# Kernel optimization log

Measured on AMD Instinct MI355X. Metric: run time of the kernel, lower is better.

## Reference

```python
import jax, jax.numpy as jnp
import numpy as np

N_WIRES = 16
VAR_DEPTH = 2
BATCH = 16


def _param_sizes():
    sizes = []
    n = N_WIRES
    lay = 0
    while n > 1:
        sizes.append(4 * int(np.ceil(N_WIRES / 2 ** lay)) * VAR_DEPTH)
        n = (n + 1) // 2
        lay += 1
    return sizes  # [128, 64, 32, 16]


def _apply_1q(psi, gate, w):
    # psi: (B, 2, ..., 2); gate: (2,2) complex; wire w lives on axis w+1
    psi = jnp.moveaxis(psi, w + 1, -1)
    psi = jnp.einsum('...j,ij->...i', psi, gate)
    return jnp.moveaxis(psi, -1, w + 1)


def _rx(psi, th, w):
    c = jnp.cos(th / 2).astype(jnp.complex64)
    s = jnp.sin(th / 2).astype(jnp.complex64)
    gate = jnp.stack([jnp.stack([c, -1j * s]), jnp.stack([-1j * s, c])])
    return _apply_1q(psi, gate, w)


def _rz(psi, th, w):
    ph = jnp.exp(0.5j * th * jnp.array([-1.0, 1.0], jnp.float32)).astype(jnp.complex64)
    shape = [1] * psi.ndim
    shape[w + 1] = 2
    return psi * ph.reshape(shape)


def _rzz(psi, th, wa, wb):
    # diag(e^{-i t/2}, e^{i t/2}, e^{i t/2}, e^{-i t/2}) -> sign = -1 if bits equal else +1
    sgn = jnp.array([[-1.0, 1.0], [1.0, -1.0]], jnp.float32)
    ph = jnp.exp(0.5j * th * sgn).astype(jnp.complex64)  # symmetric, transpose-safe
    a, b = min(wa, wb) + 1, max(wa, wb) + 1
    shape = [1] * psi.ndim
    shape[a] = 2
    shape[b] = 2
    return psi * ph.reshape(shape)


def _cnot(psi, c, t):
    p0 = jax.lax.slice_in_dim(psi, 0, 1, axis=c + 1)
    p1 = jax.lax.slice_in_dim(psi, 1, 2, axis=c + 1)
    return jnp.concatenate([p0, jnp.flip(p1, axis=t + 1)], axis=c + 1)


def _conv_layer(psi, params, active):
    n = len(active)
    for d in range(VAR_DEPTH):
        for j in range(n):
            base = 4 * j + d * 4 * n
            psi = _rx(psi, params[base + 0], active[j])
            psi = _rz(psi, params[base + 1], active[j])
            psi = _rx(psi, params[base + 2], active[j])
        for bg in (0, 1):
            for j in range(bg, n, 2):
                jn = (j + 1) % n  # ring coupling (wraps last->first)
                base = 4 * j + d * 4 * n
                psi = _rzz(psi, params[base + 3], active[j], active[jn])
    return psi


def _pool(psi, active):
    for j in range(0, len(active), 2):
        if j + 1 < len(active):
            psi = _cnot(psi, active[j], active[j + 1])
    return psi, active[::2]


def _forward(psi, params_list):
    active = list(range(N_WIRES))
    for p in params_list:
        psi = _conv_layer(psi, p, active)
        if len(active) > 1:
            psi, active = _pool(psi, active)
    w = active[0]  # measure Z on the surviving wire (wire 0)
    prob = psi.real ** 2 + psi.imag ** 2
    axes = tuple(a for a in range(1, psi.ndim) if a != w + 1)
    p2 = prob.sum(axis=axes)  # (B, 2)
    return p2[:, 0] - p2[:, 1]


def setup_inputs() -> dict:
    key = jax.random.key(0)
    ks = jax.random.split(key, 8)
    dim = 2 ** N_WIRES
    x_re = jax.random.normal(ks[0], (BATCH, dim), dtype=jnp.float32)
    x_im = jax.random.normal(ks[1], (BATCH, dim), dtype=jnp.float32)
    nrm = jnp.sqrt(jnp.sum(x_re ** 2 + x_im ** 2, axis=1, keepdims=True))
    x_re = x_re / nrm
    x_im = x_im / nrm
    sizes = _param_sizes()
    two_pi = 2.0 * np.pi
    params = [jax.random.uniform(ks[2 + i], (sizes[i],), dtype=jnp.float32) * two_pi
              for i in range(len(sizes))]
    return {"x_re": x_re, "x_im": x_im,
            "params0": params[0], "params1": params[1],
            "params2": params[2], "params3": params[3]}


def reference(x_re, x_im, params0, params1, params2, params3):
    psi = (x_re + 1j * x_im).astype(jnp.complex64)
    psi = psi.reshape((BATCH,) + (2,) * N_WIRES)
    return _forward(psi, [params0, params1, params2, params3])
```

## Files before the change

kernel.cpp:

```cpp
#include <hip/hip_runtime.h>


#define DEV __device__ __forceinline__

__device__ static const unsigned char G_CP[60] = {
  15,14,13,12,11,10,9,8,7,6,5,4,3,2,1,0,
  15,14,13,12,11,10,9,8,7,6,5,4,3,2,1,0,
  15,13,11,9,7,5,3,1,
  15,13,11,9,7,5,3,1,
  15,11,7,3,
  15,11,7,3,
  15,7,
  15,7
};
__device__ static const unsigned char G_CQ[60] = {
  14,13,12,11,10,9,8,7,6,5,4,3,2,1,0,15,
  14,13,12,11,10,9,8,7,6,5,4,3,2,1,0,15,
  13,11,9,7,5,3,1,15,
  13,11,9,7,5,3,1,15,
  11,7,3,15,
  11,7,3,15,
  7,15,
  7,15
};

DEV float2 F2(float x, float y){ float2 r; r.x = x; r.y = y; return r; }
DEV float2 cmulf(float2 a, float2 b){ return F2(a.x*b.x - a.y*b.y, a.x*b.y + a.y*b.x); }
DEV int swz(int j){ return j ^ ((j>>4)&15) ^ ((j>>8)&15); }

#if __has_builtin(__builtin_amdgcn_permlane32_swap)
#define HAVE_PLS 1
DEV void plswap01(float &x0, float &x1){
  auto r = __builtin_amdgcn_permlane32_swap(__float_as_uint(x0), __float_as_uint(x1), false, false);
  x0 = __uint_as_float((unsigned)r[0]);
  x1 = __uint_as_float((unsigned)r[1]);
}
#else
#define HAVE_PLS 0
#endif

template<int SB>
DEV void gate4(float2* a, const float* __restrict__ g){
  float u00r=g[0],u00i=g[1],u01r=g[2],u01i=g[3],u10r=g[4],u10i=g[5],u11r=g[6],u11i=g[7];
  #pragma unroll
  for (int m=0;m<2;m++){
    int i0 = (SB==0) ? (m<<1) : m;
    int i1 = i0 | (1<<SB);
    float2 x0=a[i0], x1=a[i1];
    a[i0] = F2(u00r*x0.x - u00i*x0.y + u01r*x1.x - u01i*x1.y,
               u00r*x0.y + u00i*x0.x + u01r*x1.y + u01i*x1.x);
    a[i1] = F2(u10r*x0.x - u10i*x0.y + u11r*x1.x - u11i*x1.y,
               u10r*x0.y + u10i*x0.x + u11r*x1.y + u11i*x1.x);
  }
}

DEV void lgate(float2* a, const float* __restrict__ g, int mask, int lane){
  bool h = (lane & mask) != 0;
  float Ar = h ? g[6] : g[0], Ai = h ? g[7] : g[1];
  float Br = h ? g[4] : g[2], Bi = h ? g[5] : g[3];
  #pragma unroll
  for (int s=0;s<4;s++){
    float px = __shfl_xor(a[s].x, mask);
    float py = __shfl_xor(a[s].y, mask);
    a[s] = F2(Ar*a[s].x - Ai*a[s].y + Br*px - Bi*py,
              Ar*a[s].y + Ai*a[s].x + Br*py + Bi*px);
  }
}

DEV void lgate32(float2* a, const float* __restrict__ g, int lane){
#if HAVE_PLS
  bool h = (lane & 32) != 0;
  float c0r = h ? g[4] : g[0], c0i = h ? g[5] : g[1];
  float c1r = h ? g[6] : g[2], c1i = h ? g[7] : g[3];
  #pragma unroll
  for (int s=0;s<4;s++){
    float x0x = a[s].x, x1x = a[s].x, x0y = a[s].y, x1y = a[s].y;
    plswap01(x0x, x1x); plswap01(x0y, x1y);
    a[s] = F2(c0r*x0x - c0i*x0y + c1r*x1x - c1i*x1y,
              c0r*x0y + c0i*x0x + c1r*x1y + c1i*x1x);
  }
#else
  lgate(a, g, 32, lane);
#endif
}

DEV void cswap(float2* a, int cmask, int tmask, int lane){
  bool c = (lane & cmask) != 0;
  #pragma unroll
  for (int s=0;s<4;s++){
    float px = __shfl_xor(a[s].x, tmask);
    float py = __shfl_xor(a[s].y, tmask);
    if (c){ a[s].x = px; a[s].y = py; }
  }
}

template<int C0,int N,unsigned M0,unsigned M1>
DEV void diag4(float2* a, const float* __restrict__ hh, unsigned Ib){
  const unsigned regmask = M0|M1;
  float base = 0.f;
  #pragma unroll
  for (int k=0;k<N;k++){
    const int p = G_CP[C0+k], q = G_CQ[C0+k];
    if ( !(((1u<<p)|(1u<<q)) & regmask) ){
      float h = hh[C0+k];
      unsigned x = ((Ib>>p) ^ (Ib>>q)) & 1u;
      base += x ? h : -h;
    }
  }
  #pragma unroll
  for (int r=0;r<4;r++){
    unsigned Ir = Ib ^ ((r&1)?M0:0u) ^ ((r&2)?M1:0u);
    float ph = base;
    #pragma unroll
    for (int k=0;k<N;k++){
      const int p = G_CP[C0+k], q = G_CQ[C0+k];
      if ( ((1u<<p)|(1u<<q)) & regmask ){
        float h = hh[C0+k];
        unsigned x = ((Ir>>p) ^ (Ir>>q)) & 1u;
        ph += x ? h : -h;
      }
    }
    float c, s;
    __sincosf(ph, &s, &c);
    a[r] = cmulf(a[r], F2(c, s));
  }
}

DEV void build_entry(float* sh, const float* __restrict__ p0, const float* __restrict__ p1,
                     const float* __restrict__ p2, const float* __restrict__ p3, int g){
  int d, j, n; const float* P;
  if (g < 32)      { n=16; d=(g>>4)&1; j=g&15; P=p0; }
  else if (g < 48) { n=8;  d=(g>>3)&1; j=g&7;  P=p1; }
  else if (g < 56) { n=4;  d=(g>>2)&1; j=g&3;  P=p2; }
  else             { n=2;  d=(g>>1)&1; j=g&1;  P=p3; }
  int base = 4*j + 4*n*d;
  float th0 = P[base+0], th1 = P[base+1], th2 = P[base+2], th3 = P[base+3];
  float c0,s0,ca,sa,c2,s2;
  sincosf(0.5f*th0, &s0, &c0);
  sincosf(0.5f*th1, &sa, &ca);
  sincosf(0.5f*th2, &s2, &c2);
  float B00r =  ca*c0, B00i = -sa*c0;
  float B01r = -sa*s0, B01i = -ca*s0;
  float B10r =  sa*s0, B10i = -ca*s0;
  float B11r =  ca*c0, B11i =  sa*c0;
  float* o8 = sh + g*8;
  o8[0]=c2*B00r + s2*B10i; o8[1]=c2*B00i - s2*B10r;
  o8[2]=c2*B01r + s2*B11i; o8[3]=c2*B01i - s2*B11r;
  o8[4]=s2*B00i + c2*B10r; o8[5]=-s2*B00r + c2*B10i;
  o8[6]=s2*B01i + c2*B11r; o8[7]=-s2*B01r + c2*B11i;
  sh[480 + g] = 0.5f*th3;
}

DEV unsigned Ib2(int j, int o){ return (unsigned)((j&63) | (o<<6) | ((j>>6)<<11)); }
DEV unsigned Ic(int j, int o){
  return (unsigned)( ((j&1)<<1) | (((j>>1)&1)<<3) | (((j>>2)&1)<<5)
       | (((j>>3)&63)<<6) | (((j>>9)&1)<<13) | (((j>>10)&1)<<15)
       | (o&1) | (((o>>1)&1)<<2) | (((o>>2)&1)<<4) | (((o>>3)&1)<<12) | (((o>>4)&1)<<14) );
}
DEV unsigned s1b(unsigned I){ return I ^ ((I & 0xA02Au) >> 1); }

__global__ __launch_bounds__(512, 4)
void k_p1(const float* __restrict__ xre, const float* __restrict__ xim,
          const float* __restrict__ pp0, const float* __restrict__ pp1,
          const float* __restrict__ pp2, const float* __restrict__ pp3,
          float* __restrict__ tbl, float2* __restrict__ st, float* __restrict__ out){
  const int t = threadIdx.x, lane = t & 63, wv = t >> 6;
  const int batch = blockIdx.x >> 5, o = blockIdx.x & 31;
  const unsigned hi = ((unsigned)batch<<16) | ((unsigned)o<<11);
  __shared__ float2 lds[2048];
  __shared__ float sh[544];
  float2 a[4];
  {
    unsigned base = hi | ((unsigned)t<<2);
    float4 re = *(const float4*)(xre + base);
    float4 im = *(const float4*)(xim + base);
    a[0]=F2(re.x,im.x); a[1]=F2(re.y,im.y); a[2]=F2(re.z,im.z); a[3]=F2(re.w,im.w);
  }
  if (t < 60) build_entry(sh, pp0, pp1, pp2, pp3, t);
  if (blockIdx.x == 0 && t >= 64 && t < 80) out[t - 64] = 0.f;
  __syncthreads();
  if (blockIdx.x == 0){
    for (int i = t; i < 540; i += 512) tbl[i] = sh[i];
  }
  #define LTB(i) (sh + (i)*8)
  gate4<0>(a, LTB(15)); gate4<1>(a, LTB(14));
  lgate(a, LTB(13), 1, lane);  lgate(a, LTB(12), 2, lane);
  lgate(a, LTB(11), 4, lane);  lgate(a, LTB(10), 8, lane);
  lgate(a, LTB(9), 16, lane);  lgate32(a, LTB(8), lane);
  #pragma unroll
  for (int s=0;s<4;s++) lds[swz((t<<2)|s)] = a[s];
  __syncthreads();
  #pragma unroll
  for (int s=0;s<4;s++){
    int jB = (lane&31) | (wv<<5) | (s<<8) | ((lane>>5)<<10);
    a[s] = lds[swz(jB)];
  }
  gate4<0>(a, LTB(7)); gate4<1>(a, LTB(6));
  lgate32(a, LTB(5), lane);
  #pragma unroll
  for (int s=0;s<4;s++){
    int jB = (lane&31) | (wv<<5) | (s<<8) | ((lane>>5)<<10);
    st[hi | (unsigned)jB] = a[s];
  }
  #undef LTB
}

#define TBL(i) (tbl + (i)*8)

__global__ __launch_bounds__(512, 4)
void k_p2(const float* __restrict__ tbl, float2* __restrict__ st){
  const int t = threadIdx.x, lane = t & 63, wv = t >> 6;
  const int batch = blockIdx.x >> 5, o = blockIdx.x & 31;
  const unsigned bb = (unsigned)batch<<16;
  __shared__ float2 lds[2048];
  float2 a[4];
  int jA0 = ((lane&1)<<8) | (((lane>>1)&1)<<7) | (((lane>>2)&1)<<6)
          | (((lane>>3)&1)<<0) | (((lane>>4)&1)<<1) | (((lane>>5)&1)<<2) | (wv<<3);
  #pragma unroll
  for (int s=0;s<4;s++){
    int jA = jA0 | ((s&1)<<10) | (((s>>1)&1)<<9);
    a[s] = st[bb | Ib2(jA, o)];
  }
  gate4<0>(a, TBL(0)); gate4<1>(a, TBL(1));
  lgate(a, TBL(2), 1, lane); lgate(a, TBL(3), 2, lane); lgate(a, TBL(4), 4, lane);
  diag4<0,16, (1u<<15),(1u<<14)>(a, tbl+480, Ib2(jA0, o));
  lgate(a, TBL(20), 4, lane); lgate(a, TBL(19), 2, lane); lgate(a, TBL(18), 1, lane);
  gate4<1>(a, TBL(17)); gate4<0>(a, TBL(16));
  lgate(a, TBL(31), 8, lane); lgate(a, TBL(30), 16, lane); lgate32(a, TBL(29), lane);
  #pragma unroll
  for (int s=0;s<4;s++){
    int jA = jA0 | ((s&1)<<10) | (((s>>1)&1)<<9);
    lds[swz(jA)] = a[s];
  }
  __syncthreads();
  int jB0 = (lane&7) | (((lane>>3)&1)<<5) | (wv<<6)
          | (((lane>>4)&1)<<9) | (((lane>>5)&1)<<10);
  #pragma unroll
  for (int s=0;s<4;s++){
    int jB = jB0 | ((s&1)<<3) | (((s>>1)&1)<<4);
    a[s] = lds[swz(jB)];
  }
  gate4<0>(a, TBL(28)); gate4<1>(a, TBL(27));
  lgate(a, TBL(26), 8, lane);
  #pragma unroll
  for (int s=0;s<4;s++){
    int jB = jB0 | ((s&1)<<3) | (((s>>1)&1)<<4);
    st[bb | Ib2(jB, o)] = a[s];
  }
}

__global__ __launch_bounds__(512, 4)
void k_p4(const float* __restrict__ tbl, float2* __restrict__ st, float* __restrict__ out){
  const int t = threadIdx.x, lane = t & 63, wv = t >> 6;
  const int batch = blockIdx.x >> 5, o = blockIdx.x & 31;
  const unsigned bb = (unsigned)batch<<16;
  __shared__ float2 lds[2048];
  __shared__ float red[8];
  float2 a[4];
  int jA0 = (lane&7) | (((lane>>3)&7)<<5) | (wv<<8);
  #pragma unroll
  for (int s=0;s<4;s++){
    int jA = jA0 | ((s&1)<<3) | (((s>>1)&1)<<4);
    a[s] = st[bb | s1b(Ic(jA, o))];
  }
  gate4<0>(a, TBL(25)); gate4<1>(a, TBL(24));
  lgate(a, TBL(23), 8, lane); lgate(a, TBL(22), 16, lane); lgate32(a, TBL(21), lane);
  diag4<16,16, (1u<<6),(1u<<7)>(a, tbl+480, s1b(Ic(jA0, o)));
  if (wv & 1){
#if HAVE_PLS
    #pragma unroll
    for (int s=0;s<4;s++){
      float x0x=a[s].x, x1x=a[s].x, x0y=a[s].y, x1y=a[s].y;
      plswap01(x0x, x1x); plswap01(x0y, x1y);
      a[s].x = (lane & 32) ? x0x : x1x;
      a[s].y = (lane & 32) ? x0y : x1y;
    }
#else
    #pragma unroll
    for (int s=0;s<4;s++){ a[s].x = __shfl_xor(a[s].x, 32); a[s].y = __shfl_xor(a[s].y, 32); }
#endif
  }
  cswap(a, 16, 8, lane);
  { float2 tmp=a[2]; a[2]=a[3]; a[3]=tmp; }
  #pragma unroll
  for (int s=0;s<4;s++){
    int jA = jA0 | ((s&1)<<3) | (((s>>1)&1)<<4);
    lds[swz(jA)] = a[s];
  }
  __syncthreads();
  int jB0 = ((lane&1)<<2) | (((lane>>1)&1)<<4) | (((lane>>2)&1)<<6)
          | (((lane>>3)&1)<<8) | (((lane>>4)&1)<<9) | (((lane>>5)&1)<<10)
          | ((wv&1)<<3) | (((wv>>1)&1)<<5) | (((wv>>2)&1)<<7);
  #pragma unroll
  for (int s=0;s<4;s++) a[s] = lds[swz(jB0 | (s&1) | (((s>>1)&1)<<1))];
  const unsigned IbB = Ic(jB0, o);
  gate4<0>(a, TBL(39)); gate4<1>(a, TBL(38));
  lgate(a, TBL(37), 1, lane); lgate(a, TBL(36), 2, lane); lgate(a, TBL(35), 4, lane);
  lgate(a, TBL(34), 8, lane); lgate(a, TBL(33), 16, lane); lgate32(a, TBL(32), lane);
  diag4<32,8, 2u,8u>(a, tbl+480, IbB);
  gate4<0>(a, TBL(47)); gate4<1>(a, TBL(46));
  lgate(a, TBL(45), 1, lane); lgate(a, TBL(44), 2, lane); lgate(a, TBL(43), 4, lane);
  lgate(a, TBL(42), 8, lane); lgate(a, TBL(41), 16, lane); lgate32(a, TBL(40), lane);
  diag4<40,8, 2u,8u>(a, tbl+480, IbB);
  cswap(a, 32, 16, lane); cswap(a, 8, 4, lane); cswap(a, 2, 1, lane);
  { float2 tmp=a[2]; a[2]=a[3]; a[3]=tmp; }
  lgate32(a, TBL(48), lane); lgate(a, TBL(49), 8, lane); lgate(a, TBL(50), 2, lane);
  gate4<1>(a, TBL(51));
  diag4<48,4, 2u,8u>(a, tbl+480, IbB);
  lgate32(a, TBL(52), lane); lgate(a, TBL(53), 8, lane); lgate(a, TBL(54), 2, lane);
  gate4<1>(a, TBL(55));
  diag4<52,4, 2u,8u>(a, tbl+480, IbB);
  cswap(a, 32, 8, lane);
  if (lane & 2){
    float2 t0=a[0]; a[0]=a[2]; a[2]=t0;
    float2 t1=a[1]; a[1]=a[3]; a[3]=t1;
  }
  lgate32(a, TBL(56), lane); lgate(a, TBL(57), 2, lane);
  diag4<56,2, 2u,8u>(a, tbl+480, IbB);
  lgate32(a, TBL(58), lane);
  float sl = 0.f;
  #pragma unroll
  for (int s=0;s<4;s++) sl += a[s].x*a[s].x + a[s].y*a[s].y;
  float sg = (lane & 32) ? -sl : sl;
  #pragma unroll
  for (int off=32; off>0; off>>=1) sg += __shfl_down(sg, off);
  __syncthreads();
  if ((t & 63) == 0) red[wv] = sg;
  __syncthreads();
  if (t == 0){
    float tot = 0.f;
    #pragma unroll
    for (int w=0; w<8; w++) tot += red[w];
    atomicAdd(out + batch, tot);
  }
}

extern "C" void kernel_launch(void* const* d_in, const int* in_sizes, int n_in,
                              void* d_out, int out_size, void* d_ws, size_t ws_size,
                              hipStream_t stream) {
  const float* xre = (const float*)d_in[0];
  const float* xim = (const float*)d_in[1];
  const float* p0  = (const float*)d_in[2];
  const float* p1  = (const float*)d_in[3];
  const float* p2  = (const float*)d_in[4];
  const float* p3  = (const float*)d_in[5];
  float* out = (float*)d_out;
  float2* st = (float2*)d_ws;
  float* tbl = (float*)((char*)d_ws + (8u<<20));

  k_p1<<<512, 512, 0, stream>>>(xre, xim, p0, p1, p2, p3, tbl, st, out);
  k_p2<<<512, 512, 0, stream>>>(tbl, st);
  k_p4<<<512, 512, 0, stream>>>(tbl, st, out);
}
```

Baseline: 107.6 us.

## Merge three statevector passes into two with 4096-amplitude blocks

Replaces the three kernels with two. Each block now holds 4096 amplitudes across 1024 threads, so more wires stay block-local per pass and one global round trip of the statevector is removed. The gate schedule and the RZZ diagonal phases are redistributed: diagx fuses phase groups from two layers, the LDS remaps use a new swizzle, and global loads and stores become float4. Blocks are larger with more LDS, so occupancy drops and the new bit-permutation index maps carry a correctness risk.

Measured after the change: 105.0 us. 2.4% less time.

```diff
diff --git a/kernel.cpp b/kernel.cpp
--- a/kernel.cpp
+++ b/kernel.cpp
@@ -27,6 +27,11 @@
 DEV float2 F2(float x, float y){ float2 r; r.x = x; r.y = y; return r; }
 DEV float2 cmulf(float2 a, float2 b){ return F2(a.x*b.x - a.y*b.y, a.x*b.y + a.y*b.x); }
 DEV int swz(int j){ return j ^ ((j>>4)&15) ^ ((j>>8)&15); }
+DEV int sw2(int m){
+  return m ^ ((m>>9)&1) ^ (((m>>11)&1)<<1)
+           ^ ((((m>>3)&1)^((m>>8)&1))<<2)
+           ^ ((((m>>4)&1)^((m>>5)&1)^((m>>10)&1))<<3);
+}
 
 #if __has_builtin(__builtin_amdgcn_permlane32_swap)
 #define HAVE_PLS 1
@@ -94,17 +99,24 @@
   }
 }
 
-template<int C0,int N,unsigned M0,unsigned M1>
-DEV void diag4(float2* a, const float* __restrict__ hh, unsigned Ib){
-  const unsigned regmask = M0|M1;
+template<int C0,int N0,int C1,int N1,unsigned M0,unsigned M1>
+DEV void diagx(float2* a, const float* __restrict__ hh, unsigned Ib){
+  const unsigned rm = M0|M1;
   float base = 0.f;
   #pragma unroll
-  for (int k=0;k<N;k++){
-    const int p = G_CP[C0+k], q = G_CQ[C0+k];
-    if ( !(((1u<<p)|(1u<<q)) & regmask) ){
-      float h = hh[C0+k];
-      unsigned x = ((Ib>>p) ^ (Ib>>q)) & 1u;
-      base += x ? h : -h;
+  for (int k=C0;k<C0+N0;k++){
+    const int p=G_CP[k], q=G_CQ[k];
+    if (!(((1u<<p)|(1u<<q)) & rm)){
+      float h = hh[k];
+      base += (((Ib>>p)^(Ib>>q))&1u) ? h : -h;
+    }
+  }
+  #pragma unroll
+  for (int k=C1;k<C1+N1;k++){
+    const int p=G_CP[k], q=G_CQ[k];
+    if (!(((1u<<p)|(1u<<q)) & rm)){
+      float h = hh[k];
+      base += (((Ib>>p)^(Ib>>q))&1u) ? h : -h;
     }
   }
   #pragma unroll
@@ -112,12 +124,19 @@
     unsigned Ir = Ib ^ ((r&1)?M0:0u) ^ ((r&2)?M1:0u);
     float ph = base;
     #pragma unroll
-    for (int k=0;k<N;k++){
-      const int p = G_CP[C0+k], q = G_CQ[C0+k];
-      if ( ((1u<<p)|(1u<<q)) & regmask ){
-        float h = hh[C0+k];
-        unsigned x = ((Ir>>p) ^ (Ir>>q)) & 1u;
-        ph += x ? h : -h;
+    for (int k=C0;k<C0+N0;k++){
+      const int p=G_CP[k], q=G_CQ[k];
+      if (((1u<<p)|(1u<<q)) & rm){
+        float h = hh[k];
+        ph += (((Ir>>p)^(Ir>>q))&1u) ? h : -h;
+      }
+    }
+    #pragma unroll
+    for (int k=C1;k<C1+N1;k++){
+      const int p=G_CP[k], q=G_CQ[k];
+      if (((1u<<p)|(1u<<q)) & rm){
+        float h = hh[k];
+        ph += (((Ir>>p)^(Ir>>q))&1u) ? h : -h;
       }
     }
     float c, s;
@@ -151,23 +170,15 @@
   sh[480 + g] = 0.5f*th3;
 }
 
-DEV unsigned Ib2(int j, int o){ return (unsigned)((j&63) | (o<<6) | ((j>>6)<<11)); }
-DEV unsigned Ic(int j, int o){
-  return (unsigned)( ((j&1)<<1) | (((j>>1)&1)<<3) | (((j>>2)&1)<<5)
-       | (((j>>3)&63)<<6) | (((j>>9)&1)<<13) | (((j>>10)&1)<<15)
-       | (o&1) | (((o>>1)&1)<<2) | (((o>>2)&1)<<4) | (((o>>3)&1)<<12) | (((o>>4)&1)<<14) );
-}
-DEV unsigned s1b(unsigned I){ return I ^ ((I & 0xA02Au) >> 1); }
-
-__global__ __launch_bounds__(512, 4)
-void k_p1(const float* __restrict__ xre, const float* __restrict__ xim,
+__global__ __launch_bounds__(1024, 4)
+void k_pa(const float* __restrict__ xre, const float* __restrict__ xim,
           const float* __restrict__ pp0, const float* __restrict__ pp1,
           const float* __restrict__ pp2, const float* __restrict__ pp3,
           float* __restrict__ tbl, float2* __restrict__ st, float* __restrict__ out){
   const int t = threadIdx.x, lane = t & 63, wv = t >> 6;
-  const int batch = blockIdx.x >> 5, o = blockIdx.x & 31;
-  const unsigned hi = ((unsigned)batch<<16) | ((unsigned)o<<11);
-  __shared__ float2 lds[2048];
+  const int batch = blockIdx.x >> 4, o = blockIdx.x & 15;
+  const unsigned hi = ((unsigned)batch<<16) | ((unsigned)o<<12);
+  __shared__ float2 lds[4096];
   __shared__ float sh[544];
   float2 a[4];
   {
@@ -180,157 +191,149 @@
   if (blockIdx.x == 0 && t >= 64 && t < 80) out[t - 64] = 0.f;
   __syncthreads();
   if (blockIdx.x == 0){
-    for (int i = t; i < 540; i += 512) tbl[i] = sh[i];
+    for (int i = t; i < 540; i += 1024) tbl[i] = sh[i];
   }
   #define LTB(i) (sh + (i)*8)
+  const float* HH = sh + 480;
   gate4<0>(a, LTB(15)); gate4<1>(a, LTB(14));
-  lgate(a, LTB(13), 1, lane);  lgate(a, LTB(12), 2, lane);
-  lgate(a, LTB(11), 4, lane);  lgate(a, LTB(10), 8, lane);
-  lgate(a, LTB(9), 16, lane);  lgate32(a, LTB(8), lane);
+  lgate(a, LTB(13),1,lane); lgate(a, LTB(12),2,lane);
+  lgate(a, LTB(11),4,lane); lgate(a, LTB(10),8,lane);
+  lgate(a, LTB(9),16,lane); lgate32(a, LTB(8),lane);
+  const unsigned IbA = ((unsigned)o<<12) | ((unsigned)wv<<8) | ((unsigned)lane<<2);
+  diagx<8,7,0,0,1u,2u>(a, HH, IbA);
+  gate4<1>(a, LTB(30));
+  lgate(a, LTB(29),1,lane); lgate(a, LTB(28),2,lane);
+  lgate(a, LTB(27),4,lane); lgate(a, LTB(26),8,lane);
+  lgate(a, LTB(25),16,lane);
+  diagx<25,5,0,0,1u,2u>(a, HH, IbA);
+  cswap(a,2,1,lane);
+  cswap(a,8,4,lane);
   #pragma unroll
   for (int s=0;s<4;s++) lds[swz((t<<2)|s)] = a[s];
   __syncthreads();
-  #pragma unroll
-  for (int s=0;s<4;s++){
-    int jB = (lane&31) | (wv<<5) | (s<<8) | ((lane>>5)<<10);
-    a[s] = lds[swz(jB)];
-  }
-  gate4<0>(a, LTB(7)); gate4<1>(a, LTB(6));
-  lgate32(a, LTB(5), lane);
-  #pragma unroll
-  for (int s=0;s<4;s++){
-    int jB = (lane&31) | (wv<<5) | (s<<8) | ((lane>>5)<<10);
-    st[hi | (unsigned)jB] = a[s];
+  const int idxR = (wv&15) | (((lane>>4)&1)<<4) | (((lane>>5)&1)<<5)
+                 | (((lane>>2)&1)<<6) | (((lane>>3)&1)<<7)
+                 | ((lane&1)<<8) | (((lane>>1)&1)<<9);
+  #pragma unroll
+  for (int s=0;s<4;s++) a[s] = lds[swz(idxR | ((s&1)<<10) | (((s>>1)&1)<<11))];
+  lgate(a, LTB(7),1,lane); lgate(a, LTB(6),2,lane);
+  gate4<0>(a, LTB(5)); gate4<1>(a, LTB(4));
+  const unsigned IbB = ((unsigned)o<<12) | (unsigned)idxR;
+  diagx<4,4,0,0,1024u,2048u>(a, HH, IbB);
+  lgate(a, LTB(24),8,lane);
+  lgate(a, LTB(23),1,lane); lgate(a, LTB(22),2,lane);
+  gate4<0>(a, LTB(21));
+  diagx<21,4,0,0,1024u,2048u>(a, HH, IbB);
+  cswap(a,8,4,lane);
+  cswap(a,2,1,lane);
+  {
+    unsigned sb = hi | ((unsigned)wv<<8) | ((unsigned)lane<<2);
+    float4 v0, v1;
+    v0.x=a[0].x; v0.y=a[0].y; v0.z=a[1].x; v0.w=a[1].y;
+    v1.x=a[2].x; v1.y=a[2].y; v1.z=a[3].x; v1.w=a[3].y;
+    *(float4*)(st + sb) = v0;
+    *(float4*)(st + sb + 2) = v1;
   }
   #undef LTB
 }
 
 #define TBL(i) (tbl + (i)*8)
 
-__global__ __launch_bounds__(512, 4)
-void k_p2(const float* __restrict__ tbl, float2* __restrict__ st){
+__global__ __launch_bounds__(1024, 4)
+void k_pb(const float* __restrict__ tbl, float2* __restrict__ st, float* __restrict__ out){
   const int t = threadIdx.x, lane = t & 63, wv = t >> 6;
-  const int batch = blockIdx.x >> 5, o = blockIdx.x & 31;
-  const unsigned bb = (unsigned)batch<<16;
-  __shared__ float2 lds[2048];
+  const int batch = blockIdx.x >> 4, o = blockIdx.x & 15;
+  __shared__ float2 lds[4096];
+  __shared__ float red[16];
+  const float* HH = tbl + 480;
+  const unsigned opart = ((unsigned)(o&1)<<2) | ((unsigned)((o>>1)&1)<<4)
+                       | ((unsigned)((o>>2)&1)<<6) | ((unsigned)((o>>3)&1)<<8);
   float2 a[4];
-  int jA0 = ((lane&1)<<8) | (((lane>>1)&1)<<7) | (((lane>>2)&1)<<6)
-          | (((lane>>3)&1)<<0) | (((lane>>4)&1)<<1) | (((lane>>5)&1)<<2) | (wv<<3);
-  #pragma unroll
-  for (int s=0;s<4;s++){
-    int jA = jA0 | ((s&1)<<10) | (((s>>1)&1)<<9);
-    a[s] = st[bb | Ib2(jA, o)];
-  }
-  gate4<0>(a, TBL(0)); gate4<1>(a, TBL(1));
-  lgate(a, TBL(2), 1, lane); lgate(a, TBL(3), 2, lane); lgate(a, TBL(4), 4, lane);
-  diag4<0,16, (1u<<15),(1u<<14)>(a, tbl+480, Ib2(jA0, o));
-  lgate(a, TBL(20), 4, lane); lgate(a, TBL(19), 2, lane); lgate(a, TBL(18), 1, lane);
-  gate4<1>(a, TBL(17)); gate4<0>(a, TBL(16));
-  lgate(a, TBL(31), 8, lane); lgate(a, TBL(30), 16, lane); lgate32(a, TBL(29), lane);
-  #pragma unroll
-  for (int s=0;s<4;s++){
-    int jA = jA0 | ((s&1)<<10) | (((s>>1)&1)<<9);
-    lds[swz(jA)] = a[s];
-  }
+  {
+    unsigned gb = ((unsigned)batch<<16)
+      | (((unsigned)(o>>3)&1)<<2) | (((unsigned)(o>>2)&1)<<4)
+      | (((unsigned)(o>>1)&1)<<6) | (((unsigned)o&1)<<10)
+      | (((unsigned)(wv>>3)&1)<<3) | (((unsigned)(wv>>2)&1)<<5)
+      | (((unsigned)(wv>>1)&1)<<7) | (((unsigned)wv&1)<<11)
+      | (((unsigned)(lane>>4)&1)<<8) | (((unsigned)(lane>>5)&1)<<9)
+      | (((unsigned)lane&1)<<12) | (((unsigned)(lane>>1)&1)<<13)
+      | (((unsigned)(lane>>2)&1)<<14) | (((unsigned)(lane>>3)&1)<<15);
+    const float4* sp = (const float4*)(st + gb);
+    float4 lo = sp[0], hi4 = sp[1];
+    a[0]=F2(lo.x,lo.y); a[1]=F2(lo.z,lo.w); a[2]=F2(hi4.x,hi4.y); a[3]=F2(hi4.z,hi4.w);
+  }
+  const unsigned IbA = opart
+    | (((unsigned)lane&1)<<12) | (((unsigned)(lane>>1)&1)<<13)
+    | (((unsigned)(lane>>2)&1)<<14) | (((unsigned)(lane>>3)&1)<<15)
+    | (((unsigned)(lane>>4)&1)<<0) | (((unsigned)(lane>>5)&1)<<1)
+    | (((unsigned)wv&1)<<3) | (((unsigned)(wv>>1)&1)<<5)
+    | (((unsigned)(wv>>2)&1)<<7) | (((unsigned)(wv>>3)&1)<<9);
+  lgate(a, TBL(3),1,lane); lgate(a, TBL(2),2,lane);
+  lgate(a, TBL(1),4,lane); lgate(a, TBL(0),8,lane);
+  diagx<0,4,15,1,1024u,2048u>(a, HH, IbA);
+  lgate(a, TBL(31),16,lane);
+  gate4<1>(a, TBL(20));
+  lgate(a, TBL(19),1,lane); lgate(a, TBL(18),2,lane);
+  lgate(a, TBL(17),4,lane); lgate(a, TBL(16),8,lane);
+  diagx<16,5,30,2,1024u,2048u>(a, HH, IbA);
+  cswap(a,8,4,lane);
+  cswap(a,2,1,lane);
+  { float2 tmp=a[2]; a[2]=a[3]; a[3]=tmp; }
+  cswap(a,32,16,lane);
+  const int idxW = ((lane>>4)&1) | (((lane>>5)&1)<<1)
+                 | ((wv&1)<<2) | (((wv>>1)&1)<<3) | (((wv>>2)&1)<<4) | (((wv>>3)&1)<<5)
+                 | ((lane&1)<<8) | (((lane>>1)&1)<<9)
+                 | (((lane>>2)&1)<<10) | (((lane>>3)&1)<<11);
+  #pragma unroll
+  for (int s=0;s<4;s++) lds[sw2(idxW | ((s&1)<<6) | (((s>>1)&1)<<7))] = a[s];
   __syncthreads();
-  int jB0 = (lane&7) | (((lane>>3)&1)<<5) | (wv<<6)
-          | (((lane>>4)&1)<<9) | (((lane>>5)&1)<<10);
-  #pragma unroll
-  for (int s=0;s<4;s++){
-    int jB = jB0 | ((s&1)<<3) | (((s>>1)&1)<<4);
-    a[s] = lds[swz(jB)];
-  }
-  gate4<0>(a, TBL(28)); gate4<1>(a, TBL(27));
-  lgate(a, TBL(26), 8, lane);
-  #pragma unroll
-  for (int s=0;s<4;s++){
-    int jB = jB0 | ((s&1)<<3) | (((s>>1)&1)<<4);
-    st[bb | Ib2(jB, o)] = a[s];
-  }
-}
-
-__global__ __launch_bounds__(512, 4)
-void k_p4(const float* __restrict__ tbl, float2* __restrict__ st, float* __restrict__ out){
-  const int t = threadIdx.x, lane = t & 63, wv = t >> 6;
-  const int batch = blockIdx.x >> 5, o = blockIdx.x & 31;
-  const unsigned bb = (unsigned)batch<<16;
-  __shared__ float2 lds[2048];
-  __shared__ float red[8];
-  float2 a[4];
-  int jA0 = (lane&7) | (((lane>>3)&7)<<5) | (wv<<8);
-  #pragma unroll
-  for (int s=0;s<4;s++){
-    int jA = jA0 | ((s&1)<<3) | (((s>>1)&1)<<4);
-    a[s] = st[bb | s1b(Ic(jA, o))];
-  }
-  gate4<0>(a, TBL(25)); gate4<1>(a, TBL(24));
-  lgate(a, TBL(23), 8, lane); lgate(a, TBL(22), 16, lane); lgate32(a, TBL(21), lane);
-  diag4<16,16, (1u<<6),(1u<<7)>(a, tbl+480, s1b(Ic(jA0, o)));
-  if (wv & 1){
-#if HAVE_PLS
-    #pragma unroll
-    for (int s=0;s<4;s++){
-      float x0x=a[s].x, x1x=a[s].x, x0y=a[s].y, x1y=a[s].y;
-      plswap01(x0x, x1x); plswap01(x0y, x1y);
-      a[s].x = (lane & 32) ? x0x : x1x;
-      a[s].y = (lane & 32) ? x0y : x1y;
-    }
-#else
-    #pragma unroll
-    for (int s=0;s<4;s++){ a[s].x = __shfl_xor(a[s].x, 32); a[s].y = __shfl_xor(a[s].y, 32); }
-#endif
-  }
-  cswap(a, 16, 8, lane);
+  const int idxR = (wv&1) | (((wv>>1)&1)<<6) | (((wv>>2)&1)<<8) | (((wv>>3)&1)<<10)
+                 | ((lane&1)<<3) | (((lane>>1)&1)<<4) | (((lane>>2)&1)<<5)
+                 | (((lane>>3)&1)<<7) | (((lane>>4)&1)<<9) | (((lane>>5)&1)<<11);
+  #pragma unroll
+  for (int s=0;s<4;s++) a[s] = lds[sw2(idxR | ((s&1)<<1) | (((s>>1)&1)<<2))];
+  const unsigned IbB = opart
+    | (((unsigned)wv&1)<<0) | (((unsigned)(wv>>1)&1)<<10)
+    | (((unsigned)(wv>>2)&1)<<12) | (((unsigned)(wv>>3)&1)<<14)
+    | (((unsigned)lane&1)<<5) | (((unsigned)(lane>>1)&1)<<7)
+    | (((unsigned)(lane>>2)&1)<<9) | (((unsigned)(lane>>3)&1)<<11)
+    | (((unsigned)(lane>>4)&1)<<13) | (((unsigned)(lane>>5)&1)<<15);
+  gate4<0>(a, TBL(39)); gate4<1>(a, TBL(38));
+  lgate(a, TBL(37),1,lane); lgate(a, TBL(36),2,lane); lgate(a, TBL(35),4,lane);
+  lgate(a, TBL(34),8,lane); lgate(a, TBL(33),16,lane); lgate32(a, TBL(32),lane);
+  diagx<32,8,0,0,2u,8u>(a, HH, IbB);
+  gate4<0>(a, TBL(47)); gate4<1>(a, TBL(46));
+  lgate(a, TBL(45),1,lane); lgate(a, TBL(44),2,lane); lgate(a, TBL(43),4,lane);
+  lgate(a, TBL(42),8,lane); lgate(a, TBL(41),16,lane); lgate32(a, TBL(40),lane);
+  diagx<40,8,0,0,2u,8u>(a, HH, IbB);
+  cswap(a,32,16,lane); cswap(a,8,4,lane); cswap(a,2,1,lane);
   { float2 tmp=a[2]; a[2]=a[3]; a[3]=tmp; }
-  #pragma unroll
-  for (int s=0;s<4;s++){
-    int jA = jA0 | ((s&1)<<3) | (((s>>1)&1)<<4);
-    lds[swz(jA)] = a[s];
-  }
-  __syncthreads();
-  int jB0 = ((lane&1)<<2) | (((lane>>1)&1)<<4) | (((lane>>2)&1)<<6)
-          | (((lane>>3)&1)<<8) | (((lane>>4)&1)<<9) | (((lane>>5)&1)<<10)
-          | ((wv&1)<<3) | (((wv>>1)&1)<<5) | (((wv>>2)&1)<<7);
-  #pragma unroll
-  for (int s=0;s<4;s++) a[s] = lds[swz(jB0 | (s&1) | (((s>>1)&1)<<1))];
-  const unsigned IbB = Ic(jB0, o);
-  gate4<0>(a, TBL(39)); gate4<1>(a, TBL(38));
-  lgate(a, TBL(37), 1, lane); lgate(a, TBL(36), 2, lane); lgate(a, TBL(35), 4, lane);
-  lgate(a, TBL(34), 8, lane); lgate(a, TBL(33), 16, lane); lgate32(a, TBL(32), lane);
-  diag4<32,8, 2u,8u>(a, tbl+480, IbB);
-  gate4<0>(a, TBL(47)); gate4<1>(a, TBL(46));
-  lgate(a, TBL(45), 1, lane); lgate(a, TBL(44), 2, lane); lgate(a, TBL(43), 4, lane);
-  lgate(a, TBL(42), 8, lane); lgate(a, TBL(41), 16, lane); lgate32(a, TBL(40), lane);
-  diag4<40,8, 2u,8u>(a, tbl+480, IbB);
-  cswap(a, 32, 16, lane); cswap(a, 8, 4, lane); cswap(a, 2, 1, lane);
-  { float2 tmp=a[2]; a[2]=a[3]; a[3]=tmp; }
-  lgate32(a, TBL(48), lane); lgate(a, TBL(49), 8, lane); lgate(a, TBL(50), 2, lane);
+  lgate32(a, TBL(48),lane); lgate(a, TBL(49),8,lane); lgate(a, TBL(50),2,lane);
   gate4<1>(a, TBL(51));
-  diag4<48,4, 2u,8u>(a, tbl+480, IbB);
-  lgate32(a, TBL(52), lane); lgate(a, TBL(53), 8, lane); lgate(a, TBL(54), 2, lane);
+  diagx<48,4,0,0,2u,8u>(a, HH, IbB);
+  lgate32(a, TBL(52),lane); lgate(a, TBL(53),8,lane); lgate(a, TBL(54),2,lane);
   gate4<1>(a, TBL(55));
-  diag4<52,4, 2u,8u>(a, tbl+480, IbB);
-  cswap(a, 32, 8, lane);
+  diagx<52,4,0,0,2u,8u>(a, HH, IbB);
+  cswap(a,32,8,lane);
   if (lane & 2){
     float2 t0=a[0]; a[0]=a[2]; a[2]=t0;
     float2 t1=a[1]; a[1]=a[3]; a[3]=t1;
   }
-  lgate32(a, TBL(56), lane); lgate(a, TBL(57), 2, lane);
-  diag4<56,2, 2u,8u>(a, tbl+480, IbB);
-  lgate32(a, TBL(58), lane);
+  lgate32(a, TBL(56),lane); lgate(a, TBL(57),2,lane);
+  diagx<56,2,0,0,2u,8u>(a, HH, IbB);
+  lgate32(a, TBL(58),lane);
   float sl = 0.f;
   #pragma unroll
   for (int s=0;s<4;s++) sl += a[s].x*a[s].x + a[s].y*a[s].y;
   float sg = (lane & 32) ? -sl : sl;
   #pragma unroll
   for (int off=32; off>0; off>>=1) sg += __shfl_down(sg, off);
-  __syncthreads();
   if ((t & 63) == 0) red[wv] = sg;
   __syncthreads();
   if (t == 0){
     float tot = 0.f;
     #pragma unroll
-    for (int w=0; w<8; w++) tot += red[w];
+    for (int w=0; w<16; w++) tot += red[w];
     atomicAdd(out + batch, tot);
   }
 }
@@ -348,7 +351,6 @@
   float2* st = (float2*)d_ws;
   float* tbl = (float*)((char*)d_ws + (8u<<20));
 
-  k_p1<<<512, 512, 0, stream>>>(xre, xim, p0, p1, p2, p3, tbl, st, out);
-  k_p2<<<512, 512, 0, stream>>>(tbl, st);
-  k_p4<<<512, 512, 0, stream>>>(tbl, st, out);
-}
+  k_pa<<<256, 1024, 0, stream>>>(xre, xim, p0, p1, p2, p3, tbl, st, out);
+  k_pb<<<256, 1024, 0, stream>>>(tbl, st, out);
+}
```
